# Kernel optimization log

Measured on AMD Instinct MI355X. Metric: run time of the kernel, lower is better.

The kernel has to match this reference:

```python
import jax, jax.numpy as jnp
import numpy as np

P = 16; RES = 224; D = 768; L = 12; H = 12; OUT = 512
NP1 = NP2 = RES // P          # 14x14 patches
NTOK = NP1 * NP2 + 1          # 197 tokens (cls + patches)
STD = 5.0                     # gaussian_std for naclip
EPS = 1e-5


def _ln(x, w, b):
    x32 = x.astype(jnp.float32)
    m = x32.mean(-1, keepdims=True)
    v = ((x32 - m) ** 2).mean(-1, keepdims=True)
    return (((x32 - m) * jax.lax.rsqrt(v + EPS)) * w + b).astype(x.dtype)


def _quick_gelu(x):
    return x * jax.nn.sigmoid(1.702 * x)


def _gaussian_addition():
    # VisionTransformer.gaussian_window + get_attention_addition, done analytically:
    # addition[i*NP2+j, k*NP2+l] = window[k-i+NP1-1, l-j+NP2-1]
    w1, w2 = 2 * NP1 - 1, 2 * NP2 - 1
    c = 1.0 / (STD * np.sqrt(2.0))
    k1 = (-(w1 - 1) / 2.0 + np.arange(w1)) * c
    k2 = (-(w2 - 1) / 2.0 + np.arange(w2)) * c
    window = np.exp(-(k1[:, None] ** 2 + k2[None, :] ** 2))
    r = np.arange(NP1)[None, :] - np.arange(NP1)[:, None] + (NP1 - 1)  # [i,k]
    cc = np.arange(NP2)[None, :] - np.arange(NP2)[:, None] + (NP2 - 1)  # [j,l]
    A = window[r[:, None, :, None], cc[None, :, None, :]]  # (NP1,NP2,NP1,NP2)
    A = A.reshape(NP1 * NP2, NP1 * NP2)
    full = np.zeros((NTOK, NTOK), dtype=np.float32)
    full[1:, 1:] = A  # zero row/col for cls token
    return jnp.asarray(full)


def _mha_vanilla(x, wi, bi, wo, bo):
    B, N, _ = x.shape
    hd = D // H
    qkv = x @ wi.T + bi                      # [B,N,3D]
    q, k, v = jnp.split(qkv, 3, axis=-1)
    q = q.reshape(B, N, H, hd); k = k.reshape(B, N, H, hd); v = v.reshape(B, N, H, hd)
    a = jnp.einsum('bqhd,bkhd->bhqk', q, k) * (hd ** -0.5)
    a = jax.nn.softmax(a, axis=-1)
    o = jnp.einsum('bhqk,bkhd->bqhd', a, v).reshape(B, N, D)
    return o @ wo.T + bo


def _mha_naclip(x, wi, bi, wo, bo, addition):
    B, N, _ = x.shape
    hd = D // H
    qkv = x @ wi.T + bi
    _, k, v = jnp.split(qkv, 3, axis=-1)
    k = k.reshape(B, N, H, hd); v = v.reshape(B, N, H, hd)
    a = jnp.einsum('bqhd,bkhd->bhqk', k, k) * (hd ** -0.5) + addition[None, None]
    a = jax.nn.softmax(a, axis=-1)
    o = jnp.einsum('bhqk,bkhd->bqhd', a, v).reshape(B, N, D)
    return o @ wo.T + bo


def _mlp(x, fw, fb, pw, pb):
    return _quick_gelu(x @ fw.T + fb) @ pw.T + pb


def setup_inputs() -> dict:
    key = jax.random.key(0)
    ks = jax.random.split(key, 16)
    s = D ** -0.5
    rn = lambda k, shape, sc=0.02: jax.random.normal(k, shape, jnp.float32) * sc
    return {
        'x': jax.random.normal(ks[0], (32, 3, RES, RES), jnp.float32),
        'conv1_w': rn(ks[1], (D, 3, P, P)),
        'class_embedding': rn(ks[2], (D,), s),
        'pos_embedding': rn(ks[3], (NTOK, D), s),
        'ln_pre_w': jnp.ones((D,)), 'ln_pre_b': jnp.zeros((D,)),
        'in_proj_w': rn(ks[4], (L, 3 * D, D)), 'in_proj_b': rn(ks[5], (L, 3 * D)),
        'out_proj_w': rn(ks[6], (L, D, D)), 'out_proj_b': rn(ks[7], (L, D)),
        'ln1_w': jnp.ones((L, D)), 'ln1_b': jnp.zeros((L, D)),
        'ln2_w': jnp.ones((L, D)), 'ln2_b': jnp.zeros((L, D)),
        'fc_w': rn(ks[8], (L, 4 * D, D)), 'fc_b': rn(ks[9], (L, 4 * D)),
        'cproj_w': rn(ks[10], (L, D, 4 * D)), 'cproj_b': rn(ks[11], (L, D)),
        'ln_post_w': jnp.ones((D,)), 'ln_post_b': jnp.zeros((D,)),
        'proj': rn(ks[12], (D, OUT), s),
    }


def reference(x, conv1_w, class_embedding, pos_embedding, ln_pre_w, ln_pre_b,
              in_proj_w, in_proj_b, out_proj_w, out_proj_b, ln1_w, ln1_b,
              ln2_w, ln2_b, fc_w, fc_b, cproj_w, cproj_b, ln_post_w, ln_post_b, proj):
    B = x.shape[0]
    # patch embed
    h = jax.lax.conv_general_dilated(x, conv1_w, (P, P), 'VALID',
                                     dimension_numbers=('NCHW', 'OIHW', 'NCHW'))
    h = h.reshape(B, D, NP1 * NP2).transpose(0, 2, 1)           # [B,196,D]
    cls = jnp.broadcast_to(class_embedding, (B, 1, D))
    h = jnp.concatenate([cls, h], axis=1) + pos_embedding        # [B,197,D]
    h = _ln(h, ln_pre_w, ln_pre_b)
    addition = _gaussian_addition()
    # first L-1 blocks: vanilla attention
    for i in range(L - 1):
        h = h + _mha_vanilla(_ln(h, ln1_w[i], ln1_b[i]), in_proj_w[i], in_proj_b[i],
                             out_proj_w[i], out_proj_b[i])
        h = h + _mlp(_ln(h, ln2_w[i], ln2_b[i]), fc_w[i], fc_b[i], cproj_w[i], cproj_b[i])
    # last block: naclip key-key attention with gaussian addition (arch='vanilla')
    i = L - 1
    reduced = _mha_naclip(_ln(h, ln1_w[i], ln1_b[i]), in_proj_w[i], in_proj_b[i],
                          out_proj_w[i], out_proj_b[i], addition)
    final = h + reduced
    final = final + _mlp(_ln(final, ln2_w[i], ln2_b[i]), fc_w[i], fc_b[i], cproj_w[i], cproj_b[i])
    return _ln(final, ln_post_w, ln_post_b) @ proj               # [B,197,OUT]
```

## Files before the change

kernel.cpp:

```cpp
#include <hip/hip_runtime.h>
#include <hip/hip_bf16.h>
#include <math.h>

#define BATCH 32
#define NTOK  197
#define NPATCH 196
#define DMODEL 768
#define NLAYER 12
#define NHEAD 12
#define HDIM  64
#define ROWS  (BATCH*NTOK)
#define CROWS (BATCH*NPATCH)
#define DFF   3072
#define DQKV  2304
#define DOUT  512
#define NBH   (BATCH*NHEAD)

#define WOFF_IN   ((size_t)0)
#define WOFF_OUT  ((size_t)(DQKV*DMODEL))
#define WOFF_FC   (WOFF_OUT + (size_t)(DMODEL*DMODEL))
#define WOFF_CP   (WOFF_FC + (size_t)(DFF*DMODEL))
#define WTOT      (WOFF_CP + (size_t)(DMODEL*DFF))

#define WS_H    ((size_t)0)
#define WS_QKVB (WS_H + (size_t)ROWS*DMODEL)
#define WS_GB   (WS_QKVB + (size_t)ROWS*DQKV/2)
#define WS_TB   (WS_GB + (size_t)ROWS*DFF/2)
#define WS_WL   (WS_TB + (size_t)ROWS*DMODEL/2)
#define WS_PTS  (WS_WL + WTOT/2)
#define WS_ADD  (WS_PTS + (size_t)DOUT*DMODEL/2)

typedef unsigned short ushort_t;
typedef __attribute__((ext_vector_type(8))) short bf16x8;
typedef __attribute__((ext_vector_type(4))) float f32x4;

__device__ inline ushort_t bf16rn(float x) {
    uint32_t u = __builtin_bit_cast(uint32_t, x);
    uint32_t r = (u + 0x7FFFu + ((u >> 16) & 1u)) >> 16;
    return (ushort_t)r;
}

#define GLL(src, dst) __builtin_amdgcn_global_load_lds( \
    (const __attribute__((address_space(1))) void*)(src), \
    (__attribute__((address_space(3))) void*)(dst), 16, 0, 0)


__global__ void im2col_bf16_k(const float* __restrict__ x, ushort_t* __restrict__ out) {
    int idx = blockIdx.x * 256 + threadIdx.x;
    if (idx >= CROWS * DMODEL / 4) return;
    int r  = idx / (DMODEL / 4);
    int k4 = (idx - r * (DMODEL / 4)) * 4;
    int b = r / NPATCH, p = r - b * NPATCH;
    int py = p / 14, px = p - py * 14;
    int c = k4 >> 8, rem = k4 & 255, i = rem >> 4, j = rem & 15;
    const float* xp = x + (((size_t)(b * 3 + c) * 224) + py * 16 + i) * 224 + px * 16 + j;
    float4 v = *(const float4*)xp;
    ushort4 hv = {bf16rn(v.x), bf16rn(v.y), bf16rn(v.z), bf16rn(v.w)};
    *(ushort4*)(out + (size_t)r * DMODEL + k4) = hv;
}

__global__ void cvt_w_k(const float* __restrict__ W, ushort_t* __restrict__ out, int NK) {
    int idx = (blockIdx.x * 256 + threadIdx.x) * 4;
    if (idx >= NK) return;
    float4 v = *(const float4*)(W + idx);
    ushort4 hv = {bf16rn(v.x), bf16rn(v.y), bf16rn(v.z), bf16rn(v.w)};
    *(ushort4*)(out + idx) = hv;
}

__global__ void cvt_layer_k(const float* __restrict__ inW, const float* __restrict__ outW,
                            const float* __restrict__ fcW, const float* __restrict__ cpW,
                            ushort_t* __restrict__ wl) {
    size_t idx = ((size_t)blockIdx.x * 256 + threadIdx.x) * 4;
    if (idx >= WTOT) return;
    const float* src; size_t off;
    if (idx < WOFF_OUT)      { src = inW;  off = idx; }
    else if (idx < WOFF_FC)  { src = outW; off = idx - WOFF_OUT; }
    else if (idx < WOFF_CP)  { src = fcW;  off = idx - WOFF_FC; }
    else                     { src = cpW;  off = idx - WOFF_CP; }
    float4 v = *(const float4*)(src + off);
    ushort4 hv = {bf16rn(v.x), bf16rn(v.y), bf16rn(v.z), bf16rn(v.w)};
    *(ushort4*)(wl + idx) = hv;
}

__global__ void cvt_pT_k(const float* __restrict__ proj, ushort_t* __restrict__ out) {
    int idx = blockIdx.x * 256 + threadIdx.x;
    if (idx >= DOUT * DMODEL) return;
    int n = idx / DMODEL, k = idx - n * DMODEL;
    out[(size_t)n * DMODEL + k] = bf16rn(proj[(size_t)k * DOUT + n]);
}

__global__ void embed_k(const float* __restrict__ conv, const float* __restrict__ cls,
                        const float* __restrict__ pos, float* __restrict__ h) {
    int idx = blockIdx.x * 256 + threadIdx.x;
    if (idx >= ROWS * DMODEL) return;
    int r = idx / DMODEL, d = idx - r * DMODEL;
    int b = r / NTOK, tok = r - b * NTOK;
    float v = (tok == 0) ? cls[d] : conv[((size_t)(b * NPATCH + tok - 1)) * DMODEL + d];
    h[idx] = v + pos[(size_t)tok * DMODEL + d];
}

__global__ void gauss_k(float* __restrict__ add) {
    int idx = blockIdx.x * 256 + threadIdx.x;
    if (idx >= NTOK * NTOK) return;
    int i = idx / NTOK, j = idx - i * NTOK;
    float v = 0.f;
    if (i > 0 && j > 0) {
        int p = i - 1, q = j - 1;
        int di = q / 14 - p / 14;
        int dj = q % 14 - p % 14;
        v = expf(-(float)(di * di + dj * dj) * 0.02f);
    }
    add[idx] = v;
}

__global__ __launch_bounds__(256) void ln768_k(const float* __restrict__ in, float* __restrict__ out,
                                               const float* __restrict__ w, const float* __restrict__ b) {
    int row = blockIdx.x, tid = threadIdx.x;
    const float* x = in + (size_t)row * DMODEL;
    float v0 = x[tid], v1 = x[tid + 256], v2 = x[tid + 512];
    float s = v0 + v1 + v2;
    float s2 = v0 * v0 + v1 * v1 + v2 * v2;
    for (int o = 32; o > 0; o >>= 1) { s += __shfl_down(s, o); s2 += __shfl_down(s2, o); }
    __shared__ float red[8];
    int wid = tid >> 6;
    if ((tid & 63) == 0) { red[wid] = s; red[4 + wid] = s2; }
    __syncthreads();
    s  = red[0] + red[1] + red[2] + red[3];
    s2 = red[4] + red[5] + red[6] + red[7];
    float mean = s * (1.0f / 768.0f);
    float var  = s2 * (1.0f / 768.0f) - mean * mean;
    float rinv = rsqrtf(var + 1e-5f);
    float* o_ = out + (size_t)row * DMODEL;
    o_[tid]       = (v0 - mean) * rinv * w[tid]       + b[tid];
    o_[tid + 256] = (v1 - mean) * rinv * w[tid + 256] + b[tid + 256];
    o_[tid + 512] = (v2 - mean) * rinv * w[tid + 512] + b[tid + 512];
}

__global__ __launch_bounds__(256) void ln768_bf16_k(const float* __restrict__ in, ushort_t* __restrict__ out,
                                                    const float* __restrict__ w, const float* __restrict__ b) {
    int row = blockIdx.x, tid = threadIdx.x;
    const float* x = in + (size_t)row * DMODEL;
    float v0 = x[tid], v1 = x[tid + 256], v2 = x[tid + 512];
    float s = v0 + v1 + v2;
    float s2 = v0 * v0 + v1 * v1 + v2 * v2;
    for (int o = 32; o > 0; o >>= 1) { s += __shfl_down(s, o); s2 += __shfl_down(s2, o); }
    __shared__ float red[8];
    int wid = tid >> 6;
    if ((tid & 63) == 0) { red[wid] = s; red[4 + wid] = s2; }
    __syncthreads();
    s  = red[0] + red[1] + red[2] + red[3];
    s2 = red[4] + red[5] + red[6] + red[7];
    float mean = s * (1.0f / 768.0f);
    float var  = s2 * (1.0f / 768.0f) - mean * mean;
    float rinv = rsqrtf(var + 1e-5f);
    ushort_t* o_ = out + (size_t)row * DMODEL;
    o_[tid]       = bf16rn((v0 - mean) * rinv * w[tid]       + b[tid]);
    o_[tid + 256] = bf16rn((v1 - mean) * rinv * w[tid + 256] + b[tid + 256]);
    o_[tid + 512] = bf16rn((v2 - mean) * rinv * w[tid + 512] + b[tid + 512]);
}

__global__ __launch_bounds__(256) void gemm_mfma_k(
    const ushort_t* __restrict__ A, const ushort_t* __restrict__ W,
    const float* __restrict__ bias, float* __restrict__ C, ushort_t* __restrict__ OS,
    int M, int N, int K, int mode)
{
    __shared__ ushort_t As[2][128][32];
    __shared__ ushort_t Bs[2][128][32];
    int tid = threadIdx.x;
    int lane = tid & 63;
    int wave = tid >> 6;
    int wm = wave >> 1, wn = wave & 1;
    int m0 = blockIdx.y * 128, n0 = blockIdx.x * 128;

    int klen = K / gridDim.z;
    int kbeg = blockIdx.z * klen;
    int nt = klen / 32;

    f32x4 acc[4][4];
    #pragma unroll
    for (int i = 0; i < 4; ++i)
        #pragma unroll
        for (int j = 0; j < 4; ++j)
            acc[i][j] = (f32x4){0.f, 0.f, 0.f, 0.f};

    int srow = tid >> 2;
    int skq  = (((tid & 3) ^ ((tid >> 3) & 3)) * 8);
    int ar0 = m0 + srow;      if (ar0 > M - 1) ar0 = M - 1;
    int ar1 = m0 + srow + 64; if (ar1 > M - 1) ar1 = M - 1;
    const ushort_t* Ap0 = A + (size_t)ar0 * K + kbeg + skq;
    const ushort_t* Ap1 = A + (size_t)ar1 * K + kbeg + skq;
    const ushort_t* Wp0 = W + (size_t)(n0 + srow) * K + kbeg + skq;
    const ushort_t* Wp1 = W + (size_t)(n0 + srow + 64) * K + kbeg + skq;
    char* ldsA = (char*)As + tid * 16;
    char* ldsB = (char*)Bs + tid * 16;

    int fr = lane & 15, fq = lane >> 4;
    int rsl = (fq ^ ((fr >> 1) & 3)) * 8;

    GLL(Ap0, ldsA);
    GLL(Ap1, ldsA + 4096);
    GLL(Wp0, ldsB);
    GLL(Wp1, ldsB + 4096);

    for (int t = 0; t < nt; ++t) {
        int cur = t & 1;
        if (t + 1 < nt) {
            int nx = cur ^ 1;
            size_t ko = (size_t)(t + 1) * 32;
            GLL(Ap0 + ko, ldsA + nx * 8192);
            GLL(Ap1 + ko, ldsA + nx * 8192 + 4096);
            GLL(Wp0 + ko, ldsB + nx * 8192);
            GLL(Wp1 + ko, ldsB + nx * 8192 + 4096);
            asm volatile("s_waitcnt vmcnt(4)\n\ts_barrier" ::: "memory");
        } else {
            asm volatile("s_waitcnt vmcnt(0)\n\ts_barrier" ::: "memory");
        }
        bf16x8 a[4], b[4];
        #pragma unroll
        for (int fm = 0; fm < 4; ++fm)
            a[fm] = *(const bf16x8*)&As[cur][wm * 64 + fm * 16 + fr][rsl];
        #pragma unroll
        for (int fn = 0; fn < 4; ++fn)
            b[fn] = *(const bf16x8*)&Bs[cur][wn * 64 + fn * 16 + fr][rsl];
        #pragma unroll
        for (int fm = 0; fm < 4; ++fm)
            #pragma unroll
            for (int fn = 0; fn < 4; ++fn)
                acc[fm][fn] = __builtin_amdgcn_mfma_f32_16x16x32_bf16(a[fm], b[fn], acc[fm][fn], 0, 0, 0);
        asm volatile("s_barrier" ::: "memory");
    }

    #pragma unroll
    for (int fn = 0; fn < 4; ++fn) {
        int ccol = n0 + wn * 64 + fn * 16 + fr;
        float bv = bias ? bias[ccol] : 0.f;
        if (mode == 3 && blockIdx.z != 0) bv = 0.f;
        #pragma unroll
        for (int fm = 0; fm < 4; ++fm) {
            int crow0 = m0 + wm * 64 + fm * 16 + fq * 4;
            #pragma unroll
            for (int j = 0; j < 4; ++j) {
                int row = crow0 + j;
                if (row < M) {
                    float v = acc[fm][fn][j] + bv;
                    if (mode == 0) {
                        C[(size_t)row * N + ccol] = v;
                    } else if (mode == 3) {
                        atomicAdd(&C[(size_t)row * N + ccol], v);
                    } else if (mode == 4) {
                        OS[(size_t)row * N + ccol] = bf16rn(v);
                    } else {
                        v = v / (1.0f + expf(-1.702f * v));
                        OS[(size_t)row * N + ccol] = bf16rn(v);
                    }
                }
            }
        }
    }
}

__global__ __launch_bounds__(256) void attn_fused_k(
    const ushort_t* __restrict__ qkvb, ushort_t* __restrict__ out,
    const float* __restrict__ addition, int qoff)
{
    __shared__ ushort_t Ks[208][72];
    __shared__ ushort_t Vt[64][232];
    __shared__ ushort_t Pb[4][16][40];
    int tid = threadIdx.x;
    int bh = blockIdx.x;
    int b = bh / NHEAD, hh = bh - b * NHEAD;
    const ushort_t* base = qkvb + (size_t)b * NTOK * DQKV + hh * HDIM;

    {
        int tt = tid >> 4, dq = tid & 15;
        #pragma unroll
        for (int pass = 0; pass < 13; ++pass) {
            int t = pass * 16 + tt;
            ushort4 kv = {0, 0, 0, 0}, vv = {0, 0, 0, 0};
            if (t < NTOK) {
                kv = *(const ushort4*)(base + (size_t)t * DQKV + DMODEL + dq * 4);
                vv = *(const ushort4*)(base + (size_t)t * DQKV + 2 * DMODEL + dq * 4);
            }
            *(ushort4*)&Ks[t][dq * 4] = kv;
            Vt[dq * 4 + 0][t] = vv.x;
            Vt[dq * 4 + 1][t] = vv.y;
            Vt[dq * 4 + 2][t] = vv.z;
            Vt[dq * 4 + 3][t] = vv.w;
        }
        for (int z = tid; z < 64 * 24; z += 256) Vt[z / 24][208 + z % 24] = 0;
    }
    __syncthreads();

    int lane = tid & 63, wave = tid >> 6;
    int fr = lane & 15, fq = lane >> 4;

    for (int qt = wave; qt < 13; qt += 4) {
        int i0 = qt * 16;
        int qrow = i0 + fr; if (qrow > NTOK - 1) qrow = NTOK - 1;
        const ushort_t* qp = base + (size_t)qrow * DQKV + qoff + fq * 8;
        bf16x8 q0 = *(const bf16x8*)qp;
        bf16x8 q1 = *(const bf16x8*)(qp + 32);

        f32x4 s[13];
        #pragma unroll
        for (int jt = 0; jt < 13; ++jt) {
            bf16x8 k0 = *(const bf16x8*)&Ks[jt * 16 + fr][fq * 8];
            bf16x8 k1 = *(const bf16x8*)&Ks[jt * 16 + fr][32 + fq * 8];
            f32x4 a = {0.f, 0.f, 0.f, 0.f};
            a = __builtin_amdgcn_mfma_f32_16x16x32_bf16(q0, k0, a, 0, 0, 0);
            a = __builtin_amdgcn_mfma_f32_16x16x32_bf16(q1, k1, a, 0, 0, 0);
            s[jt] = a;
        }

        int irow[4];
        #pragma unroll
        for (int jj = 0; jj < 4; ++jj) {
            int ir = i0 + fq * 4 + jj;
            irow[jj] = (ir < NTOK) ? ir : (NTOK - 1);
        }
        float m[4] = {-1e30f, -1e30f, -1e30f, -1e30f};
        #pragma unroll
        for (int jt = 0; jt < 13; ++jt) {
            int jcol = jt * 16 + fr;
            #pragma unroll
            for (int jj = 0; jj < 4; ++jj) {
                float v = s[jt][jj] * 0.125f;
                if (addition) v += addition[irow[jj] * NTOK + (jcol < NTOK ? jcol : 0)];
                if (jcol >= NTOK) v = -1e30f;
                s[jt][jj] = v;
                m[jj] = fmaxf(m[jj], v);
            }
        }
        #pragma unroll
        for (int jj = 0; jj < 4; ++jj) {
            m[jj] = fmaxf(m[jj], __shfl_xor(m[jj], 1));
            m[jj] = fmaxf(m[jj], __shfl_xor(m[jj], 2));
            m[jj] = fmaxf(m[jj], __shfl_xor(m[jj], 4));
            m[jj] = fmaxf(m[jj], __shfl_xor(m[jj], 8));
        }
        float sum[4] = {0.f, 0.f, 0.f, 0.f};
        #pragma unroll
        for (int jt = 0; jt < 13; ++jt)
            #pragma unroll
            for (int jj = 0; jj < 4; ++jj) {
                float e = __expf(s[jt][jj] - m[jj]);
                s[jt][jj] = e;
                sum[jj] += e;
            }
        #pragma unroll
        for (int jj = 0; jj < 4; ++jj) {
            sum[jj] += __shfl_xor(sum[jj], 1);
            sum[jj] += __shfl_xor(sum[jj], 2);
            sum[jj] += __shfl_xor(sum[jj], 4);
            sum[jj] += __shfl_xor(sum[jj], 8);
        }
        float inv[4];
        #pragma unroll
        for (int jj = 0; jj < 4; ++jj) inv[jj] = 1.0f / sum[jj];

        f32x4 o4[4];
        #pragma unroll
        for (int dt = 0; dt < 4; ++dt) o4[dt] = (f32x4){0.f, 0.f, 0.f, 0.f};
        for (int st = 0; st < 7; ++st) {
            #pragma unroll
            for (int half = 0; half < 2; ++half) {
                int jt = st * 2 + half;
                #pragma unroll
                for (int jj = 0; jj < 4; ++jj) {
                    ushort_t pv = 0;
                    if (jt < 13) pv = bf16rn(s[jt][jj] * inv[jj]);
                    Pb[wave][fq * 4 + jj][half * 16 + fr] = pv;
                }
            }
            asm volatile("s_waitcnt lgkmcnt(0)" ::: "memory");
            bf16x8 pa = *(const bf16x8*)&Pb[wave][fr][fq * 8];
            #pragma unroll
            for (int dt = 0; dt < 4; ++dt) {
                bf16x8 vf = *(const bf16x8*)&Vt[dt * 16 + fr][st * 32 + fq * 8];
                o4[dt] = __builtin_amdgcn_mfma_f32_16x16x32_bf16(pa, vf, o4[dt], 0, 0, 0);
            }
        }

        #pragma unroll
        for (int jj = 0; jj < 4; ++jj) {
            int ir = i0 + fq * 4 + jj;
            if (ir < NTOK) {
                ushort_t* op = out + ((size_t)(b * NTOK + ir)) * DMODEL + hh * HDIM + fr;
                #pragma unroll
                for (int dt = 0; dt < 4; ++dt)
                    op[dt * 16] = bf16rn(o4[dt][jj]);
            }
        }
    }
}

extern "C" void kernel_launch(void* const* d_in, const int* in_sizes, int n_in,
                              void* d_out, int out_size, void* d_ws, size_t ws_size,
                              hipStream_t stream) {
    const float* x        = (const float*)d_in[0];
    const float* conv1_w  = (const float*)d_in[1];
    const float* cls      = (const float*)d_in[2];
    const float* pos      = (const float*)d_in[3];
    const float* ln_pre_w = (const float*)d_in[4];
    const float* ln_pre_b = (const float*)d_in[5];
    const float* in_proj_w  = (const float*)d_in[6];
    const float* in_proj_b  = (const float*)d_in[7];
    const float* out_proj_w = (const float*)d_in[8];
    const float* out_proj_b = (const float*)d_in[9];
    const float* ln1_w = (const float*)d_in[10];
    const float* ln1_b = (const float*)d_in[11];
    const float* ln2_w = (const float*)d_in[12];
    const float* ln2_b = (const float*)d_in[13];
    const float* fc_w  = (const float*)d_in[14];
    const float* fc_b  = (const float*)d_in[15];
    const float* cproj_w = (const float*)d_in[16];
    const float* cproj_b = (const float*)d_in[17];
    const float* ln_post_w = (const float*)d_in[18];
    const float* ln_post_b = (const float*)d_in[19];
    const float* proj = (const float*)d_in[20];
    float* out = (float*)d_out;

    float* ws   = (float*)d_ws;
    float* h    = ws + WS_H;
    float* ctmp = ws + WS_QKVB;
    ushort_t* qkvb = (ushort_t*)(ws + WS_QKVB);
    ushort_t* gb   = (ushort_t*)(ws + WS_GB);
    ushort_t* tb   = (ushort_t*)(ws + WS_TB);
    ushort_t* wl   = (ushort_t*)(ws + WS_WL);
    ushort_t* pTs  = (ushort_t*)(ws + WS_PTS);
    float* add  = ws + WS_ADD;

    im2col_bf16_k<<<(CROWS * DMODEL / 4 + 255) / 256, 256, 0, stream>>>(x, tb);
    cvt_w_k<<<(DMODEL * DMODEL / 4 + 255) / 256, 256, 0, stream>>>(conv1_w, wl, DMODEL * DMODEL);
    gemm_mfma_k<<<dim3(DMODEL / 128, (CROWS + 127) / 128), 256, 0, stream>>>(
        tb, wl, nullptr, ctmp, nullptr, CROWS, DMODEL, DMODEL, 0);
    embed_k<<<(ROWS * DMODEL + 255) / 256, 256, 0, stream>>>(ctmp, cls, pos, h);
    ln768_k<<<ROWS, 256, 0, stream>>>(h, h, ln_pre_w, ln_pre_b);
    gauss_k<<<(NTOK * NTOK + 255) / 256, 256, 0, stream>>>(add);
    cvt_pT_k<<<(DOUT * DMODEL + 255) / 256, 256, 0, stream>>>(proj, pTs);

    const int GY = (ROWS + 127) / 128;
    for (int l = 0; l < NLAYER; ++l) {
        cvt_layer_k<<<(int)(WTOT / 4 / 256), 256, 0, stream>>>(
            in_proj_w + (size_t)l * DQKV * DMODEL, out_proj_w + (size_t)l * DMODEL * DMODEL,
            fc_w + (size_t)l * DFF * DMODEL, cproj_w + (size_t)l * DMODEL * DFF, wl);
        ln768_bf16_k<<<ROWS, 256, 0, stream>>>(h, tb, ln1_w + l * DMODEL, ln1_b + l * DMODEL);
        gemm_mfma_k<<<dim3(DQKV / 128, GY), 256, 0, stream>>>(
            tb, wl + WOFF_IN, in_proj_b + (size_t)l * DQKV, nullptr, qkvb, ROWS, DQKV, DMODEL, 4);
        bool nac = (l == NLAYER - 1);
        attn_fused_k<<<NBH, 256, 0, stream>>>(qkvb, tb, nac ? add : nullptr, nac ? DMODEL : 0);
        gemm_mfma_k<<<dim3(DMODEL / 128, GY, 2), 256, 0, stream>>>(
            tb, wl + WOFF_OUT, out_proj_b + (size_t)l * DMODEL, h, nullptr, ROWS, DMODEL, DMODEL, 3);
        ln768_bf16_k<<<ROWS, 256, 0, stream>>>(h, tb, ln2_w + l * DMODEL, ln2_b + l * DMODEL);
        gemm_mfma_k<<<dim3(DFF / 128, GY), 256, 0, stream>>>(
            tb, wl + WOFF_FC, fc_b + (size_t)l * DFF, nullptr, gb, ROWS, DFF, DMODEL, 1);
        gemm_mfma_k<<<dim3(DMODEL / 128, GY, 2), 256, 0, stream>>>(
            gb, wl + WOFF_CP, cproj_b + (size_t)l * DMODEL, h, nullptr, ROWS, DMODEL, DFF, 3);
    }

    ln768_bf16_k<<<ROWS, 256, 0, stream>>>(h, tb, ln_post_w, ln_post_b);
    gemm_mfma_k<<<dim3(DOUT / 128, GY), 256, 0, stream>>>(
        tb, pTs, nullptr, out, nullptr, ROWS, DOUT, DMODEL, 0);
}
```

Measured before the change: 3.540 ms.

## Restructure fused attention: 8 waves, transposed scores, double-buffered P staging

Doubles the attention block to 512 threads so each of 8 waves handles one or two query tiles. Q fragments are loaded before the K/V shared-memory fill to overlap that latency. The QK^T MFMA operands are swapped so each lane owns a whole query row, which cuts the softmax max/sum reductions to two shuffles and allows vectorized P writes. P staging is double-buffered so the next tile's writes overlap the current PV MFMAs. The cost is higher register pressure under the 512-thread launch bound, and the gain only touches attention, which is a small share of total runtime next to the GEMMs.

```diff
diff --git a/kernel.cpp b/kernel.cpp
--- a/kernel.cpp
+++ b/kernel.cpp
@@ -259,47 +259,59 @@
     }
 }
 
-__global__ __launch_bounds__(256) void attn_fused_k(
+__global__ __launch_bounds__(512, 4) void attn_fused_k(
     const ushort_t* __restrict__ qkvb, ushort_t* __restrict__ out,
     const float* __restrict__ addition, int qoff)
 {
     __shared__ ushort_t Ks[208][72];
     __shared__ ushort_t Vt[64][232];
-    __shared__ ushort_t Pb[4][16][40];
+    __shared__ ushort_t Pb[8][2][16][40];
     int tid = threadIdx.x;
     int bh = blockIdx.x;
     int b = bh / NHEAD, hh = bh - b * NHEAD;
     const ushort_t* base = qkvb + (size_t)b * NTOK * DQKV + hh * HDIM;
 
+    int lane = tid & 63, wave = tid >> 6;
+    int fr = lane & 15, fq = lane >> 4;
+    int nq = (wave + 8 < 13) ? 2 : 1;
+
+    bf16x8 qf[2][2];
+    #pragma unroll
+    for (int t = 0; t < 2; ++t) {
+        if (t < nq) {
+            int qrow = (wave + t * 8) * 16 + fr; if (qrow > NTOK - 1) qrow = NTOK - 1;
+            const ushort_t* qp = base + (size_t)qrow * DQKV + qoff + fq * 8;
+            qf[t][0] = *(const bf16x8*)qp;
+            qf[t][1] = *(const bf16x8*)(qp + 32);
+        }
+    }
+
     {
         int tt = tid >> 4, dq = tid & 15;
         #pragma unroll
-        for (int pass = 0; pass < 13; ++pass) {
-            int t = pass * 16 + tt;
-            ushort4 kv = {0, 0, 0, 0}, vv = {0, 0, 0, 0};
-            if (t < NTOK) {
-                kv = *(const ushort4*)(base + (size_t)t * DQKV + DMODEL + dq * 4);
-                vv = *(const ushort4*)(base + (size_t)t * DQKV + 2 * DMODEL + dq * 4);
+        for (int pass = 0; pass < 7; ++pass) {
+            int t = pass * 32 + tt;
+            if (t < 208) {
+                ushort4 kv = {0, 0, 0, 0}, vv = {0, 0, 0, 0};
+                if (t < NTOK) {
+                    kv = *(const ushort4*)(base + (size_t)t * DQKV + DMODEL + dq * 4);
+                    vv = *(const ushort4*)(base + (size_t)t * DQKV + 2 * DMODEL + dq * 4);
+                }
+                *(ushort4*)&Ks[t][dq * 4] = kv;
+                Vt[dq * 4 + 0][t] = vv.x;
+                Vt[dq * 4 + 1][t] = vv.y;
+                Vt[dq * 4 + 2][t] = vv.z;
+                Vt[dq * 4 + 3][t] = vv.w;
             }
-            *(ushort4*)&Ks[t][dq * 4] = kv;
-            Vt[dq * 4 + 0][t] = vv.x;
-            Vt[dq * 4 + 1][t] = vv.y;
-            Vt[dq * 4 + 2][t] = vv.z;
-            Vt[dq * 4 + 3][t] = vv.w;
-        }
-        for (int z = tid; z < 64 * 24; z += 256) Vt[z / 24][208 + z % 24] = 0;
+        }
+        for (int z = tid; z < 64 * 24; z += 512) Vt[z / 24][208 + z % 24] = 0;
     }
     __syncthreads();
 
-    int lane = tid & 63, wave = tid >> 6;
-    int fr = lane & 15, fq = lane >> 4;
-
-    for (int qt = wave; qt < 13; qt += 4) {
+    for (int t = 0; t < nq; ++t) {
+        int qt = wave + t * 8;
         int i0 = qt * 16;
-        int qrow = i0 + fr; if (qrow > NTOK - 1) qrow = NTOK - 1;
-        const ushort_t* qp = base + (size_t)qrow * DQKV + qoff + fq * 8;
-        bf16x8 q0 = *(const bf16x8*)qp;
-        bf16x8 q1 = *(const bf16x8*)(qp + 32);
+        int irow = i0 + fr; if (irow > NTOK - 1) irow = NTOK - 1;
 
         f32x4 s[13];
         #pragma unroll
@@ -307,79 +319,70 @@
             bf16x8 k0 = *(const bf16x8*)&Ks[jt * 16 + fr][fq * 8];
             bf16x8 k1 = *(const bf16x8*)&Ks[jt * 16 + fr][32 + fq * 8];
             f32x4 a = {0.f, 0.f, 0.f, 0.f};
-            a = __builtin_amdgcn_mfma_f32_16x16x32_bf16(q0, k0, a, 0, 0, 0);
-            a = __builtin_amdgcn_mfma_f32_16x16x32_bf16(q1, k1, a, 0, 0, 0);
+            a = __builtin_amdgcn_mfma_f32_16x16x32_bf16(k0, qf[t][0], a, 0, 0, 0);
+            a = __builtin_amdgcn_mfma_f32_16x16x32_bf16(k1, qf[t][1], a, 0, 0, 0);
             s[jt] = a;
         }
 
-        int irow[4];
-        #pragma unroll
-        for (int jj = 0; jj < 4; ++jj) {
-            int ir = i0 + fq * 4 + jj;
-            irow[jj] = (ir < NTOK) ? ir : (NTOK - 1);
-        }
-        float m[4] = {-1e30f, -1e30f, -1e30f, -1e30f};
+        float mx = -1e30f;
         #pragma unroll
         for (int jt = 0; jt < 13; ++jt) {
-            int jcol = jt * 16 + fr;
+            int jb = jt * 16 + fq * 4;
             #pragma unroll
             for (int jj = 0; jj < 4; ++jj) {
+                int j = jb + jj;
                 float v = s[jt][jj] * 0.125f;
-                if (addition) v += addition[irow[jj] * NTOK + (jcol < NTOK ? jcol : 0)];
-                if (jcol >= NTOK) v = -1e30f;
+                if (addition) v += addition[irow * NTOK + (j < NTOK ? j : NTOK - 1)];
+                if (j >= NTOK) v = -1e30f;
                 s[jt][jj] = v;
-                m[jj] = fmaxf(m[jj], v);
+                mx = fmaxf(mx, v);
             }
         }
-        #pragma unroll
-        for (int jj = 0; jj < 4; ++jj) {
-            m[jj] = fmaxf(m[jj], __shfl_xor(m[jj], 1));
-            m[jj] = fmaxf(m[jj], __shfl_xor(m[jj], 2));
-            m[jj] = fmaxf(m[jj], __shfl_xor(m[jj], 4));
-            m[jj] = fmaxf(m[jj], __shfl_xor(m[jj], 8));
-        }
-        float sum[4] = {0.f, 0.f, 0.f, 0.f};
+        mx = fmaxf(mx, __shfl_xor(mx, 16));
+        mx = fmaxf(mx, __shfl_xor(mx, 32));
+        float sum = 0.f;
         #pragma unroll
         for (int jt = 0; jt < 13; ++jt)
             #pragma unroll
             for (int jj = 0; jj < 4; ++jj) {
-                float e = __expf(s[jt][jj] - m[jj]);
+                float e = __expf(s[jt][jj] - mx);
                 s[jt][jj] = e;
-                sum[jj] += e;
+                sum += e;
             }
-        #pragma unroll
-        for (int jj = 0; jj < 4; ++jj) {
-            sum[jj] += __shfl_xor(sum[jj], 1);
-            sum[jj] += __shfl_xor(sum[jj], 2);
-            sum[jj] += __shfl_xor(sum[jj], 4);
-            sum[jj] += __shfl_xor(sum[jj], 8);
-        }
-        float inv[4];
-        #pragma unroll
-        for (int jj = 0; jj < 4; ++jj) inv[jj] = 1.0f / sum[jj];
+        sum += __shfl_xor(sum, 16);
+        sum += __shfl_xor(sum, 32);
+        float inv = 1.0f / sum;
 
         f32x4 o4[4];
         #pragma unroll
         for (int dt = 0; dt < 4; ++dt) o4[dt] = (f32x4){0.f, 0.f, 0.f, 0.f};
+
+        #define WRITE_P(st_, buf_) do {                                              \
+            int jA = 2 * (st_), jB = jA + 1;                                         \
+            ushort4 wa = {bf16rn(s[jA][0] * inv), bf16rn(s[jA][1] * inv),            \
+                          bf16rn(s[jA][2] * inv), bf16rn(s[jA][3] * inv)};           \
+            ushort4 wb = {0, 0, 0, 0};                                               \
+            if (jB < 13) wb = (ushort4){bf16rn(s[jB][0] * inv), bf16rn(s[jB][1] * inv), \
+                                        bf16rn(s[jB][2] * inv), bf16rn(s[jB][3] * inv)}; \
+            *(ushort4*)&Pb[wave][buf_][fr][fq * 4] = wa;                             \
+            *(ushort4*)&Pb[wave][buf_][fr][16 + fq * 4] = wb;                        \
+        } while (0)
+
+        WRITE_P(0, 0);
         for (int st = 0; st < 7; ++st) {
-            #pragma unroll
-            for (int half = 0; half < 2; ++half) {
-                int jt = st * 2 + half;
-                #pragma unroll
-                for (int jj = 0; jj < 4; ++jj) {
-                    ushort_t pv = 0;
-                    if (jt < 13) pv = bf16rn(s[jt][jj] * inv[jj]);
-                    Pb[wave][fq * 4 + jj][half * 16 + fr] = pv;
-                }
-            }
             asm volatile("s_waitcnt lgkmcnt(0)" ::: "memory");
-            bf16x8 pa = *(const bf16x8*)&Pb[wave][fr][fq * 8];
-            #pragma unroll
-            for (int dt = 0; dt < 4; ++dt) {
-                bf16x8 vf = *(const bf16x8*)&Vt[dt * 16 + fr][st * 32 + fq * 8];
-                o4[dt] = __builtin_amdgcn_mfma_f32_16x16x32_bf16(pa, vf, o4[dt], 0, 0, 0);
-            }
-        }
+            bf16x8 pa = *(const bf16x8*)&Pb[wave][st & 1][fr][fq * 8];
+            bf16x8 vf0 = *(const bf16x8*)&Vt[0 * 16 + fr][st * 32 + fq * 8];
+            bf16x8 vf1 = *(const bf16x8*)&Vt[1 * 16 + fr][st * 32 + fq * 8];
+            bf16x8 vf2 = *(const bf16x8*)&Vt[2 * 16 + fr][st * 32 + fq * 8];
+            bf16x8 vf3 = *(const bf16x8*)&Vt[3 * 16 + fr][st * 32 + fq * 8];
+            if (st < 6) WRITE_P(st + 1, (st + 1) & 1);
+            o4[0] = __builtin_amdgcn_mfma_f32_16x16x32_bf16(pa, vf0, o4[0], 0, 0, 0);
+            o4[1] = __builtin_amdgcn_mfma_f32_16x16x32_bf16(pa, vf1, o4[1], 0, 0, 0);
+            o4[2] = __builtin_amdgcn_mfma_f32_16x16x32_bf16(pa, vf2, o4[2], 0, 0, 0);
+            o4[3] = __builtin_amdgcn_mfma_f32_16x16x32_bf16(pa, vf3, o4[3], 0, 0, 0);
+        }
+        #undef WRITE_P
 
         #pragma unroll
         for (int jj = 0; jj < 4; ++jj) {
@@ -448,7 +451,7 @@
         gemm_mfma_k<<<dim3(DQKV / 128, GY), 256, 0, stream>>>(
             tb, wl + WOFF_IN, in_proj_b + (size_t)l * DQKV, nullptr, qkvb, ROWS, DQKV, DMODEL, 4);
         bool nac = (l == NLAYER - 1);
-        attn_fused_k<<<NBH, 256, 0, stream>>>(qkvb, tb, nac ? add : nullptr, nac ? DMODEL : 0);
+        attn_fused_k<<<NBH, 512, 0, stream>>>(qkvb, tb, nac ? add : nullptr, nac ? DMODEL : 0);
         gemm_mfma_k<<<dim3(DMODEL / 128, GY, 2), 256, 0, stream>>>(
             tb, wl + WOFF_OUT, out_proj_b + (size_t)l * DMODEL, h, nullptr, ROWS, DMODEL, DMODEL, 3);
         ln768_bf16_k<<<ROWS, 256, 0, stream>>>(h, tb, ln2_w + l * DMODEL, ln2_b + l * DMODEL);
```

Measured after the change: 3.585 ms. Within noise of the previous version (+1.3%).
